# Kernel tuning notes

Hardware: AMD Instinct MI355X
Metric: run time of the kernel (lower is better)

## Reference

```python
import jax, jax.numpy as jnp
import numpy as np

NUM_SENTENCES = 32
MAX_SENT_LEN = 64
EMBED_DIM = 768
BATCH = 16
TEXT_LEN = NUM_SENTENCES * MAX_SENT_LEN  # 2048


def setup_inputs() -> dict:
    key = jax.random.key(0)
    k1, k2 = jax.random.split(key)
    inputs = jax.random.normal(k1, (BATCH, TEXT_LEN, EMBED_DIM), dtype=jnp.float32)
    W = jax.random.normal(k2, (EMBED_DIM, 2 * NUM_SENTENCES), dtype=jnp.float32) * 0.02
    b = jnp.zeros((2 * NUM_SENTENCES,), dtype=jnp.float32)
    return {"inputs": inputs, "W": W, "b": b}


def reference(inputs, W, b):
    B, T, E = inputs.shape
    S, L = NUM_SENTENCES, MAX_SENT_LEN

    # offsets from mean-pooled input through Dense(2*S)
    pooled = jnp.mean(inputs, axis=1)                      # [B, E]
    offsets = pooled @ W + b                               # [B, 2S]
    # clip to [0, L-1], cast (truncation == floor for nonneg values)
    start_off = jnp.clip(offsets[:, :S], 0.0, float(L - 1)).astype(jnp.int32)  # [B, S]
    end_off = jnp.clip(offsets[:, S:], 0.0, float(L - 1)).astype(jnp.int32)    # [B, S]

    base = (jnp.arange(S, dtype=jnp.int32) * L)[None, :]   # [1, S]
    start_idx = jnp.clip(base + start_off, 0, T - L)        # [B, S]
    end_idx = jnp.clip(base + L + end_off, start_idx, T)    # [B, S]

    # vectorized slice+pad: position j of sentence i comes from start_idx+j,
    # valid while j < (end_idx - start_idx) and j < L (pad/truncate to L)
    j = jnp.arange(L, dtype=jnp.int32)                      # [L]
    gather_idx = start_idx[:, :, None] + j[None, None, :]   # [B, S, L]
    valid = j[None, None, :] < (end_idx - start_idx)[:, :, None]  # [B, S, L]

    flat_idx = jnp.clip(gather_idx, 0, T - 1).reshape(B, S * L)
    gathered = jnp.take_along_axis(inputs, flat_idx[:, :, None], axis=1)
    gathered = gathered.reshape(B, S, L, E)
    out = jnp.where(valid[:, :, :, None], gathered, jnp.zeros((), inputs.dtype))
    return out
```

## Files before the change

### kernel.cpp

```cpp
#include <hip/hip_runtime.h>

#define BATCH 16
#define T_LEN 2048
#define E_DIM 768
#define N_SENT 32
#define S_LEN 64
#define TSPLIT 16
#define TCHUNK (T_LEN / TSPLIT)

__global__ void pool_partial(const float* __restrict__ in, float* __restrict__ partial) {
    const int b  = blockIdx.x;
    const int e  = blockIdx.y * 256 + threadIdx.x;
    const int tc = blockIdx.z;
    const float* p = in + ((size_t)b * T_LEN + (size_t)tc * TCHUNK) * E_DIM + e;
    float s = 0.f;
#pragma unroll 8
    for (int t = 0; t < TCHUNK; ++t) s += p[(size_t)t * E_DIM];
    partial[((size_t)tc * BATCH + b) * E_DIM + e] = s;
}

__global__ void compute_idx(const float* __restrict__ partial,
                            const float* __restrict__ W,
                            const float* __restrict__ bias,
                            int* __restrict__ sidx, int* __restrict__ eidx) {
    __shared__ float pooled[BATCH * E_DIM];
    __shared__ int   offi[BATCH * 2 * N_SENT];
    const int tid = threadIdx.x;

    for (int i = tid; i < BATCH * E_DIM; i += 1024) {
        float s = 0.f;
#pragma unroll
        for (int t = 0; t < TSPLIT; ++t) s += partial[(size_t)t * (BATCH * E_DIM) + i];
        pooled[i] = s * (1.0f / (float)T_LEN);
    }
    __syncthreads();

    const int b = tid >> 6;
    const int c = tid & 63;
    float acc = bias[c];
    const float* pb = pooled + b * E_DIM;
#pragma unroll 8
    for (int e = 0; e < E_DIM; ++e) acc += pb[e] * W[e * (2 * N_SENT) + c];
    float cl = fminf(fmaxf(acc, 0.f), (float)(S_LEN - 1));
    offi[b * 64 + c] = (int)cl;
    __syncthreads();

    if (c < N_SENT) {
        const int so   = offi[b * 64 + c];
        const int eo   = offi[b * 64 + N_SENT + c];
        const int base = c * S_LEN;
        int si = min(base + so, T_LEN - S_LEN);
        si = max(si, 0);
        int ei = min(max(base + S_LEN + eo, si), T_LEN);
        sidx[b * N_SENT + c] = si;
        eidx[b * N_SENT + c] = ei;
    }
}

__global__ void gather_rows(const float* __restrict__ in,
                            const int* __restrict__ sidx,
                            const int* __restrict__ eidx,
                            float4* __restrict__ out) {
    const int row = blockIdx.x * 4 + threadIdx.y;
    const int j = row & (S_LEN - 1);
    const int s = (row >> 6) & (N_SENT - 1);
    const int b = row >> 11;
    const int si = sidx[b * N_SENT + s];
    const int ei = eidx[b * N_SENT + s];
    float4 v = make_float4(0.f, 0.f, 0.f, 0.f);
    if (j < ei - si) {
        int src = si + j;
        src = min(max(src, 0), T_LEN - 1);
        v = *(const float4*)(in + ((size_t)b * T_LEN + src) * E_DIM + threadIdx.x * 4);
    }
    out[(size_t)row * (E_DIM / 4) + threadIdx.x] = v;
}

extern "C" void kernel_launch(void* const* d_in, const int* in_sizes, int n_in,
                              void* d_out, int out_size, void* d_ws, size_t ws_size,
                              hipStream_t stream) {
    const float* in   = (const float*)d_in[0];
    const float* W    = (const float*)d_in[1];
    const float* bias = (const float*)d_in[2];
    float* out = (float*)d_out;

    float* partial = (float*)d_ws;
    int*   sidx    = (int*)((char*)d_ws + (size_t)TSPLIT * BATCH * E_DIM * sizeof(float));
    int*   eidx    = sidx + BATCH * N_SENT;

    pool_partial<<<dim3(BATCH, E_DIM / 256, TSPLIT), 256, 0, stream>>>(in, partial);
    compute_idx<<<1, 1024, 0, stream>>>(partial, W, bias, sidx, eidx);
    gather_rows<<<dim3(BATCH * N_SENT * S_LEN / 4), dim3(192, 4), 0, stream>>>(
        in, sidx, eidx, (float4*)out);
}
```

Measured before the change: 249.3 us.

## Vectorize pooling with float4 and parallelize index computation across batches

The pooling kernel now reads float4 per thread and splits the sequence into 32 chunks instead of 16, giving 512 blocks of 192 threads. The index computation moves from one 1024-thread block to one block per batch element, with the 768-long dot product split four ways and reduced through shared memory. The aim is to remove the serial single-block bottleneck in compute_idx and widen memory accesses in the pooling pass. It also drops redundant clamps in the gather that the index math already guarantees.

```diff
diff --git a/kernel.cpp b/kernel.cpp
--- a/kernel.cpp
+++ b/kernel.cpp
@@ -3,64 +3,80 @@
 #define BATCH 16
 #define T_LEN 2048
 #define E_DIM 768
+#define E4 (E_DIM / 4)
 #define N_SENT 32
 #define S_LEN 64
-#define TSPLIT 16
-#define TCHUNK (T_LEN / TSPLIT)
+#define NCHUNK 32
+#define ROWS_PER_CHUNK (T_LEN / NCHUNK)
 
-__global__ void pool_partial(const float* __restrict__ in, float* __restrict__ partial) {
+__global__ void pool_partial(const float4* __restrict__ in4, float4* __restrict__ partial4) {
+    const int tx = threadIdx.x;
     const int b  = blockIdx.x;
-    const int e  = blockIdx.y * 256 + threadIdx.x;
-    const int tc = blockIdx.z;
-    const float* p = in + ((size_t)b * T_LEN + (size_t)tc * TCHUNK) * E_DIM + e;
-    float s = 0.f;
+    const int tc = blockIdx.y;
+    const float4* p = in4 + ((size_t)b * T_LEN + (size_t)tc * ROWS_PER_CHUNK) * E4 + tx;
+    float4 s = make_float4(0.f, 0.f, 0.f, 0.f);
 #pragma unroll 8
-    for (int t = 0; t < TCHUNK; ++t) s += p[(size_t)t * E_DIM];
-    partial[((size_t)tc * BATCH + b) * E_DIM + e] = s;
+    for (int t = 0; t < ROWS_PER_CHUNK; ++t) {
+        float4 v = p[(size_t)t * E4];
+        s.x += v.x; s.y += v.y; s.z += v.z; s.w += v.w;
+    }
+    partial4[((size_t)tc * BATCH + b) * E4 + tx] = s;
 }
 
-__global__ void compute_idx(const float* __restrict__ partial,
+__global__ void compute_idx(const float4* __restrict__ partial4,
                             const float* __restrict__ W,
                             const float* __restrict__ bias,
                             int* __restrict__ sidx, int* __restrict__ eidx) {
-    __shared__ float pooled[BATCH * E_DIM];
-    __shared__ int   offi[BATCH * 2 * N_SENT];
+    __shared__ float pooled[E_DIM];
+    __shared__ float colsum[4][2 * N_SENT];
+    __shared__ int   offi[2 * N_SENT];
+    const int b   = blockIdx.x;
     const int tid = threadIdx.x;
 
-    for (int i = tid; i < BATCH * E_DIM; i += 1024) {
-        float s = 0.f;
+    if (tid < E4) {
+        float4 s = make_float4(0.f, 0.f, 0.f, 0.f);
 #pragma unroll
-        for (int t = 0; t < TSPLIT; ++t) s += partial[(size_t)t * (BATCH * E_DIM) + i];
-        pooled[i] = s * (1.0f / (float)T_LEN);
+        for (int tc = 0; tc < NCHUNK; ++tc) {
+            float4 v = partial4[((size_t)tc * BATCH + b) * E4 + tid];
+            s.x += v.x; s.y += v.y; s.z += v.z; s.w += v.w;
+        }
+        const float inv = 1.0f / (float)T_LEN;
+        ((float4*)pooled)[tid] = make_float4(s.x * inv, s.y * inv, s.z * inv, s.w * inv);
     }
     __syncthreads();
 
-    const int b = tid >> 6;
     const int c = tid & 63;
-    float acc = bias[c];
-    const float* pb = pooled + b * E_DIM;
+    const int q = tid >> 6;
+    float acc = 0.f;
+    const float* pb = pooled + q * 192;
+    const float* Wq = W + (size_t)q * 192 * (2 * N_SENT) + c;
 #pragma unroll 8
-    for (int e = 0; e < E_DIM; ++e) acc += pb[e] * W[e * (2 * N_SENT) + c];
-    float cl = fminf(fmaxf(acc, 0.f), (float)(S_LEN - 1));
-    offi[b * 64 + c] = (int)cl;
+    for (int e = 0; e < 192; ++e) acc += pb[e] * Wq[(size_t)e * (2 * N_SENT)];
+    colsum[q][c] = acc;
     __syncthreads();
 
-    if (c < N_SENT) {
-        const int so   = offi[b * 64 + c];
-        const int eo   = offi[b * 64 + N_SENT + c];
-        const int base = c * S_LEN;
+    if (tid < 2 * N_SENT) {
+        float o = bias[tid] + colsum[0][tid] + colsum[1][tid] + colsum[2][tid] + colsum[3][tid];
+        float cl = fminf(fmaxf(o, 0.f), (float)(S_LEN - 1));
+        offi[tid] = (int)cl;
+    }
+    __syncthreads();
+
+    if (tid < N_SENT) {
+        const int so   = offi[tid];
+        const int eo   = offi[N_SENT + tid];
+        const int base = tid * S_LEN;
         int si = min(base + so, T_LEN - S_LEN);
-        si = max(si, 0);
         int ei = min(max(base + S_LEN + eo, si), T_LEN);
-        sidx[b * N_SENT + c] = si;
-        eidx[b * N_SENT + c] = ei;
+        sidx[b * N_SENT + tid] = si;
+        eidx[b * N_SENT + tid] = ei;
     }
 }
 
-__global__ void gather_rows(const float* __restrict__ in,
+__global__ void gather_rows(const float4* __restrict__ in4,
                             const int* __restrict__ sidx,
                             const int* __restrict__ eidx,
-                            float4* __restrict__ out) {
+                            float4* __restrict__ out4) {
     const int row = blockIdx.x * 4 + threadIdx.y;
     const int j = row & (S_LEN - 1);
     const int s = (row >> 6) & (N_SENT - 1);
@@ -69,27 +85,25 @@
     const int ei = eidx[b * N_SENT + s];
     float4 v = make_float4(0.f, 0.f, 0.f, 0.f);
     if (j < ei - si) {
-        int src = si + j;
-        src = min(max(src, 0), T_LEN - 1);
-        v = *(const float4*)(in + ((size_t)b * T_LEN + src) * E_DIM + threadIdx.x * 4);
+        v = in4[((size_t)b * T_LEN + (si + j)) * E4 + threadIdx.x];
     }
-    out[(size_t)row * (E_DIM / 4) + threadIdx.x] = v;
+    out4[(size_t)row * E4 + threadIdx.x] = v;
 }
 
 extern "C" void kernel_launch(void* const* d_in, const int* in_sizes, int n_in,
                               void* d_out, int out_size, void* d_ws, size_t ws_size,
                               hipStream_t stream) {
-    const float* in   = (const float*)d_in[0];
-    const float* W    = (const float*)d_in[1];
-    const float* bias = (const float*)d_in[2];
-    float* out = (float*)d_out;
+    const float4* in4 = (const float4*)d_in[0];
+    const float*  W   = (const float*)d_in[1];
+    const float*  bias= (const float*)d_in[2];
+    float4* out4 = (float4*)d_out;
 
-    float* partial = (float*)d_ws;
-    int*   sidx    = (int*)((char*)d_ws + (size_t)TSPLIT * BATCH * E_DIM * sizeof(float));
-    int*   eidx    = sidx + BATCH * N_SENT;
+    float4* partial4 = (float4*)d_ws;
+    int* sidx = (int*)((char*)d_ws + (size_t)NCHUNK * BATCH * E4 * sizeof(float4));
+    int* eidx = sidx + BATCH * N_SENT;
 
-    pool_partial<<<dim3(BATCH, E_DIM / 256, TSPLIT), 256, 0, stream>>>(in, partial);
-    compute_idx<<<1, 1024, 0, stream>>>(partial, W, bias, sidx, eidx);
+    pool_partial<<<dim3(BATCH, NCHUNK), 192, 0, stream>>>(in4, partial4);
+    compute_idx<<<BATCH, 256, 0, stream>>>(partial4, W, bias, sidx, eidx);
     gather_rows<<<dim3(BATCH * N_SENT * S_LEN / 4), dim3(192, 4), 0, stream>>>(
-        in, sidx, eidx, (float4*)out);
+        in4, sidx, eidx, (float4*)out4);
 }
```

Result: faster. 207.1 us (-17.0%).
